# Optimization experiments

Hardware: AMD Instinct MI355X
Metric: run time of the kernel (lower is better)

The kernel has to match this reference:

```python
import jax, jax.numpy as jnp
import numpy as np

THRESHOLD = 1.0
THRESHOLD_LOW = -1.0
WINDOW = 1.0  # sinabs global `window` multiplier -> surrogate window = threshold * 1.0
BATCH = 32


@jax.custom_vjp
def threshold_subtract(v):
    # sinabs ThresholdSubtract.forward: (v > 0) * floor(v / threshold)
    return jnp.where(v > 0, jnp.floor(v / THRESHOLD), jnp.zeros_like(v))


def _ts_fwd(v):
    return threshold_subtract(v), v


def _ts_bwd(v, g):
    # surrogate gradient: pass grad where v >= threshold - window, scaled by 1/threshold
    mask = (v >= (THRESHOLD - THRESHOLD * WINDOW)).astype(g.dtype)
    return (g * mask / THRESHOLD,)


threshold_subtract.defvjp(_ts_fwd, _ts_bwd)


def setup_inputs() -> dict:
    key = jax.random.key(0)
    # (batch*time, features) = (32*1024, 1024); scale so membrane crosses threshold sometimes
    data = jax.random.normal(key, (32 * 1024, 1024), dtype=jnp.float32) * 0.8 + 0.3
    return {"data": data}


def reference(data):
    F = data.shape[-1]
    # SpikingLayer: (B*T, F) -> (B, T, F) -> (T, B, F)
    x = data.reshape(BATCH, -1, F).transpose(1, 0, 2)
    state0 = jnp.zeros(x.shape[1:], dtype=x.dtype)
    act0 = jnp.zeros_like(state0)

    def step(carry, xt):
        state, act = carry
        # membrane_reset=False: subtract membrane_subtract (== threshold) per spike
        state = xt + state - act * THRESHOLD
        # lower-bound clamp at threshold_low
        state = jax.nn.relu(state - THRESHOLD_LOW) + THRESHOLD_LOW
        act = threshold_subtract(state)
        return (state, act), act

    _, spikes = jax.lax.scan(step, (state0, act0), x)  # (T, B, F)
    # back to (B*T, F)
    return spikes.transpose(1, 0, 2).reshape(-1, F)
```

## Files before the change

### kernel.cpp

```cpp
#include <hip/hip_runtime.h>
#include <stdint.h>


constexpr int T = 1024;
constexpr int F = 1024;
constexpr int DEPTH = 16;
constexpr int NC = T / DEPTH;
constexpr int CHUNK_FLOATS = DEPTH * 64;

#define WAITVM(N) asm volatile("s_waitcnt vmcnt(" #N ")" ::: "memory")

__global__ __launch_bounds__(64) void iaf_kernel(const float* __restrict__ x,
                                                 float* __restrict__ out) {
    __shared__ float lds[4 * CHUNK_FLOATS];

    const int lane = threadIdx.x;
    const int b = blockIdx.x >> 4;
    const int f0 = (blockIdx.x & 15) * 64;

    const size_t base = ((size_t)b * T) * F + f0;
    const float* __restrict__ p = x + base;
    float* __restrict__ q = out + base + lane;

    const int lrow = lane >> 4;
    const int lcol = (lane & 15) * 4;

    float s = 0.0f, a = 0.0f;

    auto issue_chunk = [&](int k) {
        float* lb = &lds[(k & 3) * CHUNK_FLOATS];
#pragma unroll
        for (int r = 0; r < 4; ++r) {
            const float* gsrc = p + (size_t)(k * DEPTH + r * 4 + lrow) * F + lcol;
            __builtin_amdgcn_global_load_lds(
                (const __attribute__((address_space(1))) void*)gsrc,
                (__attribute__((address_space(3))) void*)(lb + r * 256),
                16, 0, 0);
        }
        __builtin_amdgcn_sched_barrier(0);
    };

    auto compute_chunk = [&](int k) {
        const float* lb = &lds[(k & 3) * CHUNK_FLOATS];
        float xv[DEPTH];
#pragma unroll
        for (int i = 0; i < DEPTH; ++i) xv[i] = lb[i * 64 + lane];
#pragma unroll
        for (int i = 0; i < DEPTH; ++i) {
            s = (xv[i] + s) - a;
            s = fmaxf(s + 1.0f, 0.0f) - 1.0f;
            a = (s > 0.0f) ? floorf(s) : 0.0f;
            q[(size_t)(k * DEPTH + i) * F] = a;
        }
    };

    issue_chunk(0);
    issue_chunk(1);
    issue_chunk(2);

    WAITVM(8);  issue_chunk(3); compute_chunk(0);
    WAITVM(24); issue_chunk(4); compute_chunk(1);
    WAITVM(40); issue_chunk(5); compute_chunk(2);

    for (int c = 3; c <= 61; ++c) {
        WAITVM(56);
        if (c <= 60) issue_chunk(c + 3);
        compute_chunk(c);
    }

    WAITVM(48); compute_chunk(62);
    WAITVM(48); compute_chunk(63);
}

extern "C" void kernel_launch(void* const* d_in, const int* in_sizes, int n_in,
                              void* d_out, int out_size, void* d_ws, size_t ws_size,
                              hipStream_t stream) {
    const float* x = (const float*)d_in[0];
    float* out = (float*)d_out;
    iaf_kernel<<<dim3(512), dim3(64), 0, stream>>>(x, out);
}
```

Before: 44.58 us.

## Deepen LDS prefetch ring and stage output through LDS for float4 stores

```diff
diff --git a/kernel.cpp b/kernel.cpp
--- a/kernel.cpp
+++ b/kernel.cpp
@@ -1,18 +1,21 @@
 #include <hip/hip_runtime.h>
-#include <stdint.h>
 
 
 constexpr int T = 1024;
 constexpr int F = 1024;
-constexpr int DEPTH = 16;
+constexpr int DEPTH = 32;
 constexpr int NC = T / DEPTH;
-constexpr int CHUNK_FLOATS = DEPTH * 64;
+constexpr int CH = DEPTH * 64;
+constexpr int RING = 6;
 
 #define WAITVM(N) asm volatile("s_waitcnt vmcnt(" #N ")" ::: "memory")
+#define LGKM0()   asm volatile("s_waitcnt lgkmcnt(0)" ::: "memory")
+#define SFENCE()  __builtin_amdgcn_sched_barrier(0)
 
 __global__ __launch_bounds__(64) void iaf_kernel(const float* __restrict__ x,
                                                  float* __restrict__ out) {
-    __shared__ float lds[4 * CHUNK_FLOATS];
+    __shared__ float ring[RING * CH];
+    __shared__ float outT[DEPTH * 64];
 
     const int lane = threadIdx.x;
     const int b = blockIdx.x >> 4;
@@ -20,56 +23,67 @@
 
     const size_t base = ((size_t)b * T) * F + f0;
     const float* __restrict__ p = x + base;
-    float* __restrict__ q = out + base + lane;
+    float* __restrict__ qo = out + base;
 
     const int lrow = lane >> 4;
     const int lcol = (lane & 15) * 4;
 
     float s = 0.0f, a = 0.0f;
 
-    auto issue_chunk = [&](int k) {
-        float* lb = &lds[(k & 3) * CHUNK_FLOATS];
+    auto issue = [&](int k, int rb) {
+        float* lb = &ring[rb * CH];
 #pragma unroll
-        for (int r = 0; r < 4; ++r) {
-            const float* gsrc = p + (size_t)(k * DEPTH + r * 4 + lrow) * F + lcol;
+        for (int r = 0; r < 8; ++r) {
+            const float* g = p + (size_t)(k * DEPTH + r * 4 + lrow) * F + lcol;
             __builtin_amdgcn_global_load_lds(
-                (const __attribute__((address_space(1))) void*)gsrc,
+                (const __attribute__((address_space(1))) void*)g,
                 (__attribute__((address_space(3))) void*)(lb + r * 256),
                 16, 0, 0);
         }
-        __builtin_amdgcn_sched_barrier(0);
+        SFENCE();
     };
 
-    auto compute_chunk = [&](int k) {
-        const float* lb = &lds[(k & 3) * CHUNK_FLOATS];
-        float xv[DEPTH];
-#pragma unroll
-        for (int i = 0; i < DEPTH; ++i) xv[i] = lb[i * 64 + lane];
+    auto compute = [&](int k, int rb) {
+        const float* lb = &ring[rb * CH];
 #pragma unroll
         for (int i = 0; i < DEPTH; ++i) {
-            s = (xv[i] + s) - a;
+            const float xv = lb[i * 64 + lane];
+            s = (xv + s) - a;
             s = fmaxf(s + 1.0f, 0.0f) - 1.0f;
-            a = (s > 0.0f) ? floorf(s) : 0.0f;
-            q[(size_t)(k * DEPTH + i) * F] = a;
+            a = floorf(fmaxf(s, 0.0f));
+            outT[i * 64 + lane] = a;
         }
+        LGKM0();
+        SFENCE();
+#pragma unroll
+        for (int j = 0; j < 8; ++j) {
+            const int row = j * 4 + lrow;
+            const float4 v = *(const float4*)&outT[row * 64 + lcol];
+            *(float4*)(qo + (size_t)(k * DEPTH + row) * F + lcol) = v;
+        }
+        SFENCE();
     };
 
-    issue_chunk(0);
-    issue_chunk(1);
-    issue_chunk(2);
+    issue(0, 0); issue(1, 1); issue(2, 2); issue(3, 3);
 
-    WAITVM(8);  issue_chunk(3); compute_chunk(0);
-    WAITVM(24); issue_chunk(4); compute_chunk(1);
-    WAITVM(40); issue_chunk(5); compute_chunk(2);
+    WAITVM(24); issue(4, 4); compute(0, 0);
+    WAITVM(32); issue(5, 5); compute(1, 1);
+    WAITVM(40); issue(6, 0); compute(2, 2);
+    WAITVM(48); issue(7, 1); compute(3, 3);
 
-    for (int c = 3; c <= 61; ++c) {
+    int bc = 4, bl = 2;
+    for (int c = 4; c <= 27; ++c) {
         WAITVM(56);
-        if (c <= 60) issue_chunk(c + 3);
-        compute_chunk(c);
+        issue(c + 4, bl);
+        compute(c, bc);
+        bc = (bc == RING - 1) ? 0 : bc + 1;
+        bl = (bl == RING - 1) ? 0 : bl + 1;
     }
 
-    WAITVM(48); compute_chunk(62);
-    WAITVM(48); compute_chunk(63);
+    WAITVM(56); compute(28, 4);
+    WAITVM(48); compute(29, 5);
+    WAITVM(40); compute(30, 0);
+    WAITVM(32); compute(31, 1);
 }
 
 extern "C" void kernel_launch(void* const* d_in, const int* in_sizes, int n_in,
```

After: 50.98 us. 1.14x slower.
